# Kernel optimization log

Measured on AMD Instinct MI355X. Metric: run time of the kernel, lower is better.

Reference implementation:

```python
import jax, jax.numpy as jnp
import numpy as np

PLACEHOLDER_TOKEN_ID = -1


def setup_inputs() -> dict:
    key = jax.random.key(0)
    ks = jax.random.split(key, 7)
    B, S, V = 64, 4, 128000
    target_logits = jax.random.normal(ks[0], (B, S, V), dtype=jnp.float32)
    draft_probs = jax.random.uniform(ks[1], (B, S, V), dtype=jnp.float32)
    draft_probs = draft_probs / draft_probs.sum(axis=-1, keepdims=True)  # valid prob dist
    draft_token_ids = jax.random.randint(ks[2], (B, S), 0, V)
    bonus_token_ids = jax.random.randint(ks[3], (B,), 0, V)
    top_k = jax.random.randint(ks[4], (B,), 0, 4)  # top_k==1 -> greedy request
    uniform_probs = jax.random.uniform(ks[5], (B, S), dtype=jnp.float32)
    u = jax.random.uniform(ks[6], (B, V), dtype=jnp.float32, minval=1e-6, maxval=1.0)
    inv_q = -1.0 / jnp.log(u)  # 1 / Exponential(1) sample
    return {"target_logits": target_logits, "draft_probs": draft_probs,
            "draft_token_ids": draft_token_ids, "bonus_token_ids": bonus_token_ids,
            "top_k": top_k, "uniform_probs": uniform_probs, "inv_q": inv_q}


def _rejection_sample(target_logits, draft_probs, draft_token_ids, bonus_token_ids,
                      top_k, uniform_probs, inv_q):
    B, S, V = target_logits.shape
    is_greedy = (top_k == 1)  # [B]

    # ---- greedy path: accept while draft matches target argmax ----
    target_argmax = jnp.argmax(target_logits, axis=-1)  # [B, S]
    mismatch = draft_token_ids != target_argmax  # [B, S]
    mm = mismatch.astype(jnp.int32)
    rejected_before_g = (jnp.cumsum(mm, axis=1) - mm) > 0  # exclusive prefix
    greedy_tokens = jnp.where(rejected_before_g, PLACEHOLDER_TOKEN_ID, target_argmax)
    greedy_bonus = jnp.where(mismatch.any(axis=1), PLACEHOLDER_TOKEN_ID, bonus_token_ids)
    greedy_out = jnp.concatenate([greedy_tokens, greedy_bonus[:, None]], axis=1)

    # ---- random path: accept if target_prob/draft_prob >= uniform ----
    target_probs = jax.nn.softmax(target_logits.astype(jnp.float32), axis=-1)  # [B,S,V]
    d_at = jnp.take_along_axis(draft_probs, draft_token_ids[..., None], axis=-1)[..., 0]
    t_at = jnp.take_along_axis(target_probs, draft_token_ids[..., None], axis=-1)[..., 0]
    ratio = jnp.where(d_at > 0, t_at / jnp.where(d_at > 0, d_at, 1.0), 0.0)
    accept = (d_at > 0) & (ratio >= uniform_probs)  # [B, S]

    # recovered tokens via Gumbel-max: argmax of max(target-draft,0) * inv_q
    score = jnp.maximum(target_probs - draft_probs, 0.0) * inv_q[:, None, :]  # [B,S,V]
    recovered = jnp.argmax(score, axis=-1)  # [B, S]

    rand_tok = jnp.where(accept, draft_token_ids, recovered)
    rej = (~accept).astype(jnp.int32)
    rejected_before_r = (jnp.cumsum(rej, axis=1) - rej) > 0
    rand_tokens = jnp.where(rejected_before_r, PLACEHOLDER_TOKEN_ID, rand_tok)
    rand_bonus = jnp.where((~accept).any(axis=1), PLACEHOLDER_TOKEN_ID, bonus_token_ids)
    rand_out = jnp.concatenate([rand_tokens, rand_bonus[:, None]], axis=1)

    output_token_ids = jnp.where(is_greedy[:, None], greedy_out, rand_out)  # [B, S+1]

    # ---- extract outputs ----
    valid = output_token_ids != PLACEHOLDER_TOKEN_ID
    num_accepted = valid.sum(axis=1)  # always >= 1
    num_rejected_tokens = (S + 1) - num_accepted
    last_token_ids = jnp.take_along_axis(output_token_ids, (num_accepted - 1)[:, None], axis=1)[:, 0]
    return output_token_ids, num_rejected_tokens, last_token_ids


def reference(target_logits, draft_probs, draft_token_ids, bonus_token_ids,
              top_k, uniform_probs, inv_q):
    return _rejection_sample(target_logits, draft_probs, draft_token_ids,
                             bonus_token_ids, top_k, uniform_probs, inv_q)
```

## Files before the change

kernel.cpp:

```cpp
#include <hip/hip_runtime.h>
#include <math.h>
#include <limits.h>

#define NCHUNK 16
#define PLACEHOLDER (-1)

typedef float f32x4 __attribute__((ext_vector_type(4)));

__device__ __forceinline__ float fexp(float x) {
  return exp2f(fmaf(x, 1.44269504088896340736f, -23.0831206542234143f));
}

__device__ __forceinline__ void comb_mx(float& m, int& i, float m2, int i2) {
  if (m2 > m || (m2 == m && i2 < i)) { m = m2; i = i2; }
}

__device__ __forceinline__ int accept_row(
    const float* __restrict__ logits, const float* __restrict__ draft,
    const int* __restrict__ dids, const float* __restrict__ uniform,
    const float* __restrict__ ps, int row, int V, float& Zout) {
  float Z = 0.f;
#pragma unroll
  for (int c = 0; c < NCHUNK; ++c) Z += ps[row * NCHUNK + c];
  Zout = Z;
  const int tok = dids[row];
  const float t_at = fexp(logits[(size_t)row * V + tok]) / Z;
  const float d_at = draft[(size_t)row * V + tok];
  const float u = uniform[row];
  return (d_at > 0.f && (t_at / d_at) >= u) ? 1 : 0;
}

__global__ __launch_bounds__(256) void k_stats(
    const float* __restrict__ logits, const int* __restrict__ topk,
    float* __restrict__ pm, float* __restrict__ ps, int* __restrict__ pidx,
    int S, int V, int chunk_elems) {
  const int row = blockIdx.y;
  const int chunk = blockIdx.x;
  const int tid = threadIdx.x;
  const int b = row / S;
  const int begin = chunk * chunk_elems;
  const int end = min(begin + chunk_elems, V);
  const int n = max(end - begin, 0);
  const int c4 = n >> 2;
  const float* lrow = logits + (size_t)row * V;
  const f32x4* l4 = (const f32x4*)(lrow + begin);
  const int item = row * NCHUNK + chunk;

  __shared__ float shf[4];
  __shared__ int shi[4];
  const int lane = tid & 63;
  const int wv = tid >> 6;

  if (topk[b] == 1) {
    float m = -INFINITY; int mi = INT_MAX;
    for (int i = tid; i < c4; i += 256) {
      f32x4 v = l4[i];
      const int gi = begin + (i << 2);
#pragma unroll
      for (int k = 0; k < 4; ++k)
        if (v[k] > m) { m = v[k]; mi = gi + k; }
    }
    for (int j = begin + (c4 << 2) + tid; j < end; j += 256) {
      float x = lrow[j];
      if (x > m) { m = x; mi = j; }
    }
    for (int off = 32; off; off >>= 1) {
      float m2 = __shfl_xor(m, off);
      int   i2 = __shfl_xor(mi, off);
      comb_mx(m, mi, m2, i2);
    }
    if (lane == 0) { shf[wv] = m; shi[wv] = mi; }
    __syncthreads();
    if (tid == 0) {
#pragma unroll
      for (int w = 1; w < 4; ++w) comb_mx(m, mi, shf[w], shi[w]);
      pm[item] = m; pidx[item] = mi;
    }
  } else {
    float ssum = 0.f;
    for (int i = tid; i < c4; i += 256) {
      f32x4 v = l4[i];
      ssum += fexp(v[0]); ssum += fexp(v[1]);
      ssum += fexp(v[2]); ssum += fexp(v[3]);
    }
    for (int j = begin + (c4 << 2) + tid; j < end; j += 256)
      ssum += fexp(lrow[j]);
    for (int off = 32; off; off >>= 1)
      ssum += __shfl_xor(ssum, off);
    if (lane == 0) shf[wv] = ssum;
    __syncthreads();
    if (tid == 0)
      ps[item] = shf[0] + shf[1] + shf[2] + shf[3];
  }
}

__global__ __launch_bounds__(256) void k_score(
    const float* __restrict__ logits, const float* __restrict__ draft,
    const float* __restrict__ invq, const int* __restrict__ topk,
    const int* __restrict__ dids, const float* __restrict__ uniform,
    const float* __restrict__ ps,
    int S, int V, int chunk_elems,
    float* __restrict__ psm, int* __restrict__ psi) {
  const int row = blockIdx.y;
  const int b = row / S;
  if (topk[b] == 1) return;
  const int tid = threadIdx.x;
  const int chunk = blockIdx.x;
  const int item = row * NCHUNK + chunk;
  const int ownS = row - b * S;

  __shared__ float sInvZ;
  __shared__ int sGo;
  if (tid < 64) {
    int a = 1; float Z = 1.f;
    if (tid < S)
      a = accept_row(logits, draft, dids, uniform, ps, b * S + tid, V, Z);
    unsigned long long rej = __ballot(a == 0);
    int first = rej ? (int)__ffsll(rej) - 1 : -1;
    if (tid == 0) sGo = (first == ownS);
    if (tid == ownS) sInvZ = 1.0f / Z;
  }
  __syncthreads();
  if (!sGo) return;
  const float invZ = sInvZ;

  const int begin = chunk * chunk_elems;
  const int end = min(begin + chunk_elems, V);
  const int n = max(end - begin, 0);
  const int c4 = n >> 2;
  const float* lrow = logits + (size_t)row * V;
  const float* drow = draft + (size_t)row * V;
  const float* qrow = invq + (size_t)b * V;
  const f32x4* l4 = (const f32x4*)(lrow + begin);
  const f32x4* d4 = (const f32x4*)(drow + begin);
  const f32x4* q4 = (const f32x4*)(qrow + begin);

  __shared__ float shf[4];
  __shared__ int shi[4];
  float smx = -INFINITY; int si = INT_MAX;
  for (int i = tid; i < c4; i += 256) {
    f32x4 lv = l4[i];
    f32x4 dv = __builtin_nontemporal_load(d4 + i);
    f32x4 qv = q4[i];
    const int gi = begin + (i << 2);
#pragma unroll
    for (int k = 0; k < 4; ++k) {
      float p = fexp(lv[k]) * invZ;
      float sc = fmaxf(p - dv[k], 0.f) * qv[k];
      if (sc > smx) { smx = sc; si = gi + k; }
    }
  }
  for (int j = begin + (c4 << 2) + tid; j < end; j += 256) {
    float p = fexp(lrow[j]) * invZ;
    float sc = fmaxf(p - drow[j], 0.f) * qrow[j];
    if (sc > smx) { smx = sc; si = j; }
  }

  const int lane = tid & 63;
  const int wv = tid >> 6;
  for (int off = 32; off; off >>= 1) {
    float m2 = __shfl_xor(smx, off);
    int   i2 = __shfl_xor(si, off);
    comb_mx(smx, si, m2, i2);
  }
  if (lane == 0) { shf[wv] = smx; shi[wv] = si; }
  __syncthreads();
  if (tid == 0) {
#pragma unroll
    for (int w = 1; w < 4; ++w) comb_mx(smx, si, shf[w], shi[w]);
    psm[item] = smx; psi[item] = si;
  }
}

__global__ __launch_bounds__(64) void k_finalize(
    const float* __restrict__ logits, const float* __restrict__ draft,
    const int* __restrict__ dids, const int* __restrict__ bonus,
    const int* __restrict__ topk, const float* __restrict__ uniform,
    const float* __restrict__ pm, const int* __restrict__ pidx,
    const float* __restrict__ ps,
    const float* __restrict__ psm, const int* __restrict__ psi,
    int B, int S, int V, int* __restrict__ out) {
  const int b = blockIdx.x;
  const int lane = threadIdx.x;
  const bool greedy = (topk[b] == 1);

  __shared__ int tam[8];
  __shared__ int sFirst, sAccMask;

  if (greedy) {
    if (lane < S) {
      const int row = b * S + lane;
      float m = -INFINITY; int mi = INT_MAX;
#pragma unroll
      for (int c = 0; c < NCHUNK; ++c)
        comb_mx(m, mi, pm[row * NCHUNK + c], pidx[row * NCHUNK + c]);
      tam[lane] = mi;
    }
  } else {
    int a = 1; float Z;
    if (lane < S)
      a = accept_row(logits, draft, dids, uniform, ps, b * S + lane, V, Z);
    unsigned long long rej = __ballot(a == 0);
    unsigned long long accm = __ballot(a != 0);
    if (lane == 0) {
      sFirst = rej ? (int)__ffsll(rej) - 1 : -1;
      sAccMask = (int)(accm & ((1u << S) - 1));
    }
  }
  __syncthreads();

  if (lane == 0) {
    int tokv[9];
    bool rejected_before = false, any_rej = false;
    int first = greedy ? -1 : sFirst;
    int rectok = 0;
    if (!greedy && first >= 0) {
      const int row = b * S + first;
      float m = -INFINITY; int mi = INT_MAX;
#pragma unroll
      for (int c = 0; c < NCHUNK; ++c)
        comb_mx(m, mi, psm[row * NCHUNK + c], psi[row * NCHUNK + c]);
      rectok = mi;
    }
    for (int ss = 0; ss < S; ++ss) {
      const int r = b * S + ss;
      const int dtok = dids[r];
      int t; bool rej;
      if (greedy) {
        const int ta = tam[ss];
        rej = (dtok != ta);
        t = ta;
      } else {
        rej = (ss == first);
        t = rej ? rectok : dtok;
      }
      tokv[ss] = rejected_before ? PLACEHOLDER : t;
      any_rej = any_rej || rej;
      rejected_before = rejected_before || rej;
    }
    tokv[S] = any_rej ? PLACEHOLDER : bonus[b];
    int na = 0;
    const int Sp1 = S + 1;
    for (int j = 0; j < Sp1; ++j) na += (tokv[j] != PLACEHOLDER);
    for (int j = 0; j < Sp1; ++j) out[b * Sp1 + j] = tokv[j];
    out[B * Sp1 + b] = Sp1 - na;
    out[B * Sp1 + B + b] = tokv[na - 1];
  }
}

extern "C" void kernel_launch(void* const* d_in, const int* in_sizes, int n_in,
                              void* d_out, int out_size, void* d_ws, size_t ws_size,
                              hipStream_t stream) {
  const float* logits = (const float*)d_in[0];
  const float* draft  = (const float*)d_in[1];
  const int*   dids   = (const int*)d_in[2];
  const int*   bonus  = (const int*)d_in[3];
  const int*   topk   = (const int*)d_in[4];
  const float* unif   = (const float*)d_in[5];
  const float* invq   = (const float*)d_in[6];
  int* out = (int*)d_out;

  const int B = in_sizes[3];
  const int S = in_sizes[2] / B;
  const int V = in_sizes[0] / in_sizes[2];
  const int nrows = B * S;
  const int nitems = nrows * NCHUNK;

  char* w = (char*)d_ws;
  float* pm   = (float*)w; w += (size_t)nitems * sizeof(float);
  float* ps   = (float*)w; w += (size_t)nitems * sizeof(float);
  int*   pidx = (int*)w;   w += (size_t)nitems * sizeof(int);
  float* psm  = (float*)w; w += (size_t)nitems * sizeof(float);
  int*   psi  = (int*)w;   w += (size_t)nitems * sizeof(int);

  int chunk_elems = (V + NCHUNK - 1) / NCHUNK;
  chunk_elems = (chunk_elems + 3) & ~3;

  dim3 grid1(NCHUNK, nrows);
  k_stats<<<grid1, dim3(256), 0, stream>>>(logits, topk, pm, ps, pidx,
                                           S, V, chunk_elems);
  k_score<<<grid1, dim3(256), 0, stream>>>(
      logits, draft, invq, topk, dids, unif, ps, S, V, chunk_elems, psm, psi);
  k_finalize<<<dim3(B), dim3(64), 0, stream>>>(
      logits, draft, dids, bonus, topk, unif, pm, pidx, ps, psm, psi,
      B, S, V, out);
}
```

Measured before the change: 47.44 us.

## Fuse finalize into score kernel using atomic max and last-block completion

Removes the separate finalize launch. The score kernel now writes the output for greedy and all-accept rows directly. For rejected rows it merges per-chunk argmax results through a packed 64-bit atomicMax and a per-batch completion counter, and the last-arriving block emits the output. This saves a kernel launch and a pass over partial buffers, at the cost of atomics and fences on the critical path. The inv_q loads are also switched to nontemporal.

```diff
diff --git a/kernel.cpp b/kernel.cpp
--- a/kernel.cpp
+++ b/kernel.cpp
@@ -6,6 +6,7 @@
 #define PLACEHOLDER (-1)
 
 typedef float f32x4 __attribute__((ext_vector_type(4)));
+typedef unsigned long long u64;
 
 __device__ __forceinline__ float fexp(float x) {
   return exp2f(fmaf(x, 1.44269504088896340736f, -23.0831206542234143f));
@@ -33,6 +34,7 @@
 __global__ __launch_bounds__(256) void k_stats(
     const float* __restrict__ logits, const int* __restrict__ topk,
     float* __restrict__ pm, float* __restrict__ ps, int* __restrict__ pidx,
+    u64* __restrict__ slot, int* __restrict__ done,
     int S, int V, int chunk_elems) {
   const int row = blockIdx.y;
   const int chunk = blockIdx.x;
@@ -46,6 +48,11 @@
   const f32x4* l4 = (const f32x4*)(lrow + begin);
   const int item = row * NCHUNK + chunk;
 
+  if (chunk == 0 && tid == 0) {
+    slot[row] = 0ull;
+    if (row == b * S) done[b] = 0;
+  }
+
   __shared__ float shf[4];
   __shared__ int shi[4];
   const int lane = tid & 63;
@@ -97,33 +104,98 @@
 __global__ __launch_bounds__(256) void k_score(
     const float* __restrict__ logits, const float* __restrict__ draft,
     const float* __restrict__ invq, const int* __restrict__ topk,
-    const int* __restrict__ dids, const float* __restrict__ uniform,
-    const float* __restrict__ ps,
-    int S, int V, int chunk_elems,
-    float* __restrict__ psm, int* __restrict__ psi) {
+    const int* __restrict__ dids, const int* __restrict__ bonus,
+    const float* __restrict__ uniform, const float* __restrict__ ps,
+    const float* __restrict__ pm, const int* __restrict__ pidx,
+    u64* __restrict__ slot, int* __restrict__ done,
+    int B, int S, int V, int chunk_elems, int* __restrict__ out) {
   const int row = blockIdx.y;
+  const int chunk = blockIdx.x;
+  const int tid = threadIdx.x;
   const int b = row / S;
-  if (topk[b] == 1) return;
-  const int tid = threadIdx.x;
-  const int chunk = blockIdx.x;
-  const int item = row * NCHUNK + chunk;
   const int ownS = row - b * S;
-
+  const bool greedy = (topk[b] == 1);
+  const int Sp1 = S + 1;
+
+  __shared__ int sRole;
   __shared__ float sInvZ;
-  __shared__ int sGo;
+  __shared__ int sFirst;
+  __shared__ float shf[4];
+  __shared__ int shi[4];
+  __shared__ int sLast;
+  __shared__ int tam[8];
+
   if (tid < 64) {
-    int a = 1; float Z = 1.f;
-    if (tid < S)
-      a = accept_row(logits, draft, dids, uniform, ps, b * S + tid, V, Z);
-    unsigned long long rej = __ballot(a == 0);
-    int first = rej ? (int)__ffsll(rej) - 1 : -1;
-    if (tid == 0) sGo = (first == ownS);
-    if (tid == ownS) sInvZ = 1.0f / Z;
+    if (greedy) {
+      if (tid == 0) sRole = (chunk == 0 && ownS == 0) ? 2 : 0;
+    } else {
+      int a = 1; float Z = 1.f;
+      if (tid < S)
+        a = accept_row(logits, draft, dids, uniform, ps, b * S + tid, V, Z);
+      unsigned long long rej = __ballot(a == 0);
+      int first = rej ? (int)__ffsll(rej) - 1 : -1;
+      if (tid == ownS) sInvZ = 1.0f / Z;
+      if (tid == 0) {
+        sFirst = first;
+        sRole = (first >= 0) ? (ownS == first ? 1 : 0)
+                             : ((chunk == 0 && ownS == 0) ? 3 : 0);
+      }
+    }
   }
   __syncthreads();
-  if (!sGo) return;
+  const int role = sRole;
+  if (role == 0) return;
+
+  if (role == 2) {
+    if (tid < 64) {
+      const int s = tid >> 4;
+      const int c = tid & 15;
+      float m = -INFINITY; int mi = INT_MAX;
+      if (s < S) {
+        const int oo = (b * S + s) * NCHUNK + c;
+        m = pm[oo]; mi = pidx[oo];
+      }
+      for (int off = 8; off; off >>= 1) {
+        float m2 = __shfl_xor(m, off);
+        int   i2 = __shfl_xor(mi, off);
+        comb_mx(m, mi, m2, i2);
+      }
+      if (c == 0 && s < S) tam[s] = mi;
+    }
+    __syncthreads();
+    if (tid == 0) {
+      int tokv[9];
+      bool rejected_before = false, any_rej = false;
+      for (int ss = 0; ss < S; ++ss) {
+        const int dtok = dids[b * S + ss];
+        const int ta = tam[ss];
+        const bool rej = (dtok != ta);
+        tokv[ss] = rejected_before ? PLACEHOLDER : ta;
+        any_rej = any_rej || rej;
+        rejected_before = rejected_before || rej;
+      }
+      tokv[S] = any_rej ? PLACEHOLDER : bonus[b];
+      int na = 0;
+      for (int j = 0; j < Sp1; ++j) na += (tokv[j] != PLACEHOLDER);
+      for (int j = 0; j < Sp1; ++j) out[b * Sp1 + j] = tokv[j];
+      out[B * Sp1 + b] = Sp1 - na;
+      out[B * Sp1 + B + b] = tokv[na - 1];
+    }
+    return;
+  }
+
+  if (role == 3) {
+    if (tid == 0) {
+      for (int ss = 0; ss < S; ++ss) out[b * Sp1 + ss] = dids[b * S + ss];
+      const int bt = bonus[b];
+      out[b * Sp1 + S] = bt;
+      out[B * Sp1 + b] = 0;
+      out[B * Sp1 + B + b] = bt;
+    }
+    return;
+  }
+
   const float invZ = sInvZ;
-
   const int begin = chunk * chunk_elems;
   const int end = min(begin + chunk_elems, V);
   const int n = max(end - begin, 0);
@@ -135,13 +207,11 @@
   const f32x4* d4 = (const f32x4*)(drow + begin);
   const f32x4* q4 = (const f32x4*)(qrow + begin);
 
-  __shared__ float shf[4];
-  __shared__ int shi[4];
   float smx = -INFINITY; int si = INT_MAX;
   for (int i = tid; i < c4; i += 256) {
     f32x4 lv = l4[i];
     f32x4 dv = __builtin_nontemporal_load(d4 + i);
-    f32x4 qv = q4[i];
+    f32x4 qv = __builtin_nontemporal_load(q4 + i);
     const int gi = begin + (i << 2);
 #pragma unroll
     for (int k = 0; k < 4; ++k) {
@@ -168,83 +238,26 @@
   if (tid == 0) {
 #pragma unroll
     for (int w = 1; w < 4; ++w) comb_mx(smx, si, shf[w], shi[w]);
-    psm[item] = smx; psi[item] = si;
-  }
-}
-
-__global__ __launch_bounds__(64) void k_finalize(
-    const float* __restrict__ logits, const float* __restrict__ draft,
-    const int* __restrict__ dids, const int* __restrict__ bonus,
-    const int* __restrict__ topk, const float* __restrict__ uniform,
-    const float* __restrict__ pm, const int* __restrict__ pidx,
-    const float* __restrict__ ps,
-    const float* __restrict__ psm, const int* __restrict__ psi,
-    int B, int S, int V, int* __restrict__ out) {
-  const int b = blockIdx.x;
-  const int lane = threadIdx.x;
-  const bool greedy = (topk[b] == 1);
-
-  __shared__ int tam[8];
-  __shared__ int sFirst, sAccMask;
-
-  if (greedy) {
-    if (lane < S) {
-      const int row = b * S + lane;
-      float m = -INFINITY; int mi = INT_MAX;
-#pragma unroll
-      for (int c = 0; c < NCHUNK; ++c)
-        comb_mx(m, mi, pm[row * NCHUNK + c], pidx[row * NCHUNK + c]);
-      tam[lane] = mi;
-    }
-  } else {
-    int a = 1; float Z;
-    if (lane < S)
-      a = accept_row(logits, draft, dids, uniform, ps, b * S + lane, V, Z);
-    unsigned long long rej = __ballot(a == 0);
-    unsigned long long accm = __ballot(a != 0);
-    if (lane == 0) {
-      sFirst = rej ? (int)__ffsll(rej) - 1 : -1;
-      sAccMask = (int)(accm & ((1u << S) - 1));
-    }
+    const u64 key = ((u64)__float_as_uint(smx) << 32) | (unsigned)(~si);
+    atomicMax(&slot[row], key);
+    __threadfence();
+    const int old = __hip_atomic_fetch_add(&done[b], 1, __ATOMIC_ACQ_REL,
+                                           __HIP_MEMORY_SCOPE_AGENT);
+    sLast = (old == NCHUNK - 1);
   }
   __syncthreads();
-
-  if (lane == 0) {
-    int tokv[9];
-    bool rejected_before = false, any_rej = false;
-    int first = greedy ? -1 : sFirst;
-    int rectok = 0;
-    if (!greedy && first >= 0) {
-      const int row = b * S + first;
-      float m = -INFINITY; int mi = INT_MAX;
-#pragma unroll
-      for (int c = 0; c < NCHUNK; ++c)
-        comb_mx(m, mi, psm[row * NCHUNK + c], psi[row * NCHUNK + c]);
-      rectok = mi;
-    }
-    for (int ss = 0; ss < S; ++ss) {
-      const int r = b * S + ss;
-      const int dtok = dids[r];
-      int t; bool rej;
-      if (greedy) {
-        const int ta = tam[ss];
-        rej = (dtok != ta);
-        t = ta;
-      } else {
-        rej = (ss == first);
-        t = rej ? rectok : dtok;
-      }
-      tokv[ss] = rejected_before ? PLACEHOLDER : t;
-      any_rej = any_rej || rej;
-      rejected_before = rejected_before || rej;
-    }
-    tokv[S] = any_rej ? PLACEHOLDER : bonus[b];
-    int na = 0;
-    const int Sp1 = S + 1;
-    for (int j = 0; j < Sp1; ++j) na += (tokv[j] != PLACEHOLDER);
-    for (int j = 0; j < Sp1; ++j) out[b * Sp1 + j] = tokv[j];
-    out[B * Sp1 + b] = Sp1 - na;
-    out[B * Sp1 + B + b] = tokv[na - 1];
+  if (sLast && tid == 0) {
+    __threadfence();
+    const u64 key = __hip_atomic_load(&slot[row], __ATOMIC_ACQUIRE,
+                                      __HIP_MEMORY_SCOPE_AGENT);
+    const int rec = ~(int)(unsigned)(key & 0xFFFFFFFFull);
+    const int first = sFirst;
+    for (int ss = 0; ss < S; ++ss)
+      out[b * Sp1 + ss] = (ss < first) ? dids[b * S + ss]
+                        : (ss == first ? rec : PLACEHOLDER);
+    out[b * Sp1 + S] = PLACEHOLDER;
+    out[B * Sp1 + b] = S - first;
+    out[B * Sp1 + B + b] = rec;
   }
 }
 
@@ -270,18 +283,16 @@
   float* pm   = (float*)w; w += (size_t)nitems * sizeof(float);
   float* ps   = (float*)w; w += (size_t)nitems * sizeof(float);
   int*   pidx = (int*)w;   w += (size_t)nitems * sizeof(int);
-  float* psm  = (float*)w; w += (size_t)nitems * sizeof(float);
-  int*   psi  = (int*)w;   w += (size_t)nitems * sizeof(int);
+  u64*   slot = (u64*)w;   w += (size_t)nrows * sizeof(u64);
+  int*   done = (int*)w;   w += (size_t)B * sizeof(int);
 
   int chunk_elems = (V + NCHUNK - 1) / NCHUNK;
   chunk_elems = (chunk_elems + 3) & ~3;
 
   dim3 grid1(NCHUNK, nrows);
   k_stats<<<grid1, dim3(256), 0, stream>>>(logits, topk, pm, ps, pidx,
-                                           S, V, chunk_elems);
+                                           slot, done, S, V, chunk_elems);
   k_score<<<grid1, dim3(256), 0, stream>>>(
-      logits, draft, invq, topk, dids, unif, ps, S, V, chunk_elems, psm, psi);
-  k_finalize<<<dim3(B), dim3(64), 0, stream>>>(
-      logits, draft, dids, bonus, topk, unif, pm, pidx, ps, psm, psi,
-      B, S, V, out);
-}
+      logits, draft, invq, topk, dids, bonus, unif, ps, pm, pidx,
+      slot, done, B, S, V, chunk_elems, out);
+}
```

Result: slower. 89.64 us (+88.9%).
